# Performance work log

Measured on AMD Instinct MI355X. Metric: run time of the kernel, lower is better.

Reference implementation:

```python
import jax, jax.numpy as jnp
import numpy as np

B = 16384          # batch size
S = 7              # grid size (hard-coded in original)
IMG = 448.0        # image size (hard-coded)
CELL = IMG / S     # 64.0 pixels per cell
LAMBDA_COORD = 5.0
LAMBDA_NOOBJ = 0.5


def setup_inputs() -> dict:
    key = jax.random.key(0)
    k1, k2, k3 = jax.random.split(key, 3)
    # predictions: raw head output [B, 30, 7, 7]; keep >= 0.05 so sqrt(w), sqrt(h) are safe
    input_ = jax.random.uniform(k1, (B, 30, S, S), jnp.float32, 0.05, 1.0)
    # targets already channels-last [B, 7, 7, 30]
    target = jax.random.uniform(k2, (B, S, S, 30), jnp.float32, 0.05, 1.0)
    # objectness channel must be exactly 1.0 where an object exists (code tests == 1)
    conf = (jax.random.uniform(k3, (B, S, S)) < 0.25).astype(jnp.float32)
    target = target.at[..., 4].set(conf)
    return {"input_": input_, "target": target}


def _grid_offsets(dtype):
    # flattened [B*49] pixel offsets of each cell's top-left corner
    g = jnp.arange(S, dtype=dtype)
    gx = jnp.broadcast_to(g[None, :], (S, S)).reshape(-1) * CELL  # varies with column
    gy = jnp.broadcast_to(g[:, None], (S, S)).reshape(-1) * CELL  # varies with row
    return jnp.tile(gx, B), jnp.tile(gy, B)


def _decode_box(p, c, gx, gy):
    # p: [N,30]; box at columns c..c+4 -> clamped corner coords in pixels
    cx = p[:, c] * CELL + gx
    cy = p[:, c + 1] * CELL + gy
    w = p[:, c + 2] * IMG
    h = p[:, c + 3] * IMG
    x1 = jnp.clip(cx - w * 0.5, 0.0, IMG)
    y1 = jnp.clip(cy - h * 0.5, 0.0, IMG)
    x2 = jnp.clip(cx + w * 0.5, 0.0, IMG)
    y2 = jnp.clip(cy + h * 0.5, 0.0, IMG)
    return x1, y1, x2, y2


def _iou(a, b):
    ax1, ay1, ax2, ay2 = a
    bx1, by1, bx2, by2 = b
    l = jnp.maximum(ax1, bx1)
    r = jnp.minimum(ax2, bx2)
    t = jnp.maximum(ay1, by1)
    bo = jnp.minimum(ay2, by2)
    m = (l < r) & (t < bo)
    inter = (r - l) * (bo - t)
    union = (ax2 - ax1) * (ay2 - ay1) + (bx2 - bx1) * (by2 - by1)
    denom = union - inter
    return jnp.where(m, inter / jnp.where(m, denom, 1.0), 0.0)


def _yolo_loss(input_, target):
    # [B,30,7,7] -> [B,7,7,30] -> [N,30]
    x = jnp.transpose(input_, (0, 2, 3, 1)).reshape(-1, 30)
    t = target.reshape(-1, 30)
    gx, gy = _grid_offsets(x.dtype)

    iou1 = _iou(_decode_box(x, 0, gx, gy), _decode_box(t, 0, gx, gy))
    iou2 = _iou(_decode_box(x, 5, gx, gy), _decode_box(t, 5, gx, gy))
    mask = iou1 < iou2                      # True -> second predicted box is responsible
    iou = jnp.where(mask, iou2, iou1)

    sel = jnp.where(mask[:, None], x[:, 5:10], x[:, :5])  # responsible box [N,5]
    w = (t[:, 4] == 1.0).astype(x.dtype)                   # hasObj as 0/1 weights

    coord = jnp.sum(w * ((sel[:, 0] - t[:, 0]) ** 2 + (sel[:, 1] - t[:, 1]) ** 2))
    size = jnp.sum(w * ((jnp.sqrt(sel[:, 2]) - jnp.sqrt(t[:, 2])) ** 2
                        + (jnp.sqrt(sel[:, 3]) - jnp.sqrt(t[:, 3])) ** 2))
    conf = jnp.sum(w * (sel[:, 4] - iou) ** 2)
    noobj = jnp.sum((1.0 - w) * sel[:, 4] ** 2)
    cls = jnp.sum(w[:, None] * (x[:, 10:] - t[:, 10:]) ** 2)

    return (LAMBDA_COORD * coord + LAMBDA_COORD * size + conf
            + LAMBDA_NOOBJ * noobj + cls)


def reference(input_, target):
    return _yolo_loss(input_, target)
```

## Files before the change

kernel.cpp:

```cpp
#include <hip/hip_runtime.h>


#define NCH     30
#define CELLS   49
#define TPB     256
#define WB      6
#define BATCH_F 1470
#define STAGE_F (WB * BATCH_F)
#define STAGE_CHUNKS (STAGE_F / 4)
#define IMGSZ   448.0f
#define CELLSZ  64.0f

__device__ __forceinline__ float iou_f(float ax1, float ay1, float ax2, float ay2,
                                       float bx1, float by1, float bx2, float by2) {
    float l  = fmaxf(ax1, bx1);
    float r  = fminf(ax2, bx2);
    float t  = fmaxf(ay1, by1);
    float bo = fminf(ay2, by2);
    bool  m  = (l < r) && (t < bo);
    float inter = (r - l) * (bo - t);
    float uni   = (ax2 - ax1) * (ay2 - ay1) + (bx2 - bx1) * (by2 - by1);
    float denom = uni - inter;
    return m ? (inter / denom) : 0.0f;
}

__device__ __forceinline__ void decode_box(float p0, float p1, float p2, float p3,
                                           float gx, float gy,
                                           float& x1, float& y1, float& x2, float& y2) {
    float cx = p0 * CELLSZ + gx;
    float cy = p1 * CELLSZ + gy;
    float w  = p2 * IMGSZ;
    float h  = p3 * IMGSZ;
    x1 = fminf(fmaxf(cx - w * 0.5f, 0.0f), IMGSZ);
    y1 = fminf(fmaxf(cy - h * 0.5f, 0.0f), IMGSZ);
    x2 = fminf(fmaxf(cx + w * 0.5f, 0.0f), IMGSZ);
    y2 = fminf(fmaxf(cy + h * 0.5f, 0.0f), IMGSZ);
}

__global__ __launch_bounds__(TPB) void yolo_loss_kernel(
        const float* __restrict__ input,
        const float* __restrict__ target,
        float* __restrict__ out,
        int nbatch) {
    __shared__ __align__(16) float s_in[STAGE_F];
    __shared__ __align__(16) float s_tg[STAGE_F];
    __shared__ float red[TPB / 64];

    const int tid = threadIdx.x;
    const int b0  = blockIdx.x * WB;
    const int nb  = min(WB, nbatch - b0);
    const int nchunks = (nb * BATCH_F) >> 2;

    const float* gin = input  + (long long)b0 * BATCH_F;
    const float* gtg = target + (long long)b0 * BATCH_F;
    #pragma unroll
    for (int k = 0; k < (STAGE_CHUNKS + TPB - 1) / TPB; ++k) {
        int i = k * TPB + tid;
        if (i < nchunks) {
            __builtin_amdgcn_global_load_lds(
                (const __attribute__((address_space(1))) unsigned int*)(gin + i * 4),
                (__attribute__((address_space(3))) unsigned int*)(&s_in[i * 4]),
                16, 0, 0);
            __builtin_amdgcn_global_load_lds(
                (const __attribute__((address_space(1))) unsigned int*)(gtg + i * 4),
                (__attribute__((address_space(3))) unsigned int*)(&s_tg[i * 4]),
                16, 0, 0);
        }
    }
    __syncthreads();

    const int ncell = nb * CELLS;
    float loss = 0.0f;
    for (int local = tid; local < ncell; local += TPB) {
        const int bb  = local / CELLS;
        const int s   = local - bb * CELLS;
        const int row = s / 7;
        const int col = s - row * 7;
        const float gx = (float)col * CELLSZ;
        const float gy = (float)row * CELLSZ;

        const float* __restrict__ tl = &s_tg[local * NCH];
        const float* __restrict__ ipx = &s_in[bb * BATCH_F + s];

        float x[NCH];
        #pragma unroll
        for (int c = 0; c < NCH; ++c) x[c] = ipx[c * CELLS];

        float p0x1, p0y1, p0x2, p0y2, p1x1, p1y1, p1x2, p1y2;
        decode_box(x[0], x[1], x[2], x[3], gx, gy, p0x1, p0y1, p0x2, p0y2);
        decode_box(x[5], x[6], x[7], x[8], gx, gy, p1x1, p1y1, p1x2, p1y2);
        float t0x1, t0y1, t0x2, t0y2, t1x1, t1y1, t1x2, t1y2;
        decode_box(tl[0], tl[1], tl[2], tl[3], gx, gy, t0x1, t0y1, t0x2, t0y2);
        decode_box(tl[5], tl[6], tl[7], tl[8], gx, gy, t1x1, t1y1, t1x2, t1y2);

        float iou1 = iou_f(p0x1, p0y1, p0x2, p0y2, t0x1, t0y1, t0x2, t0y2);
        float iou2 = iou_f(p1x1, p1y1, p1x2, p1y2, t1x1, t1y1, t1x2, t1y2);

        bool  mask = iou1 < iou2;
        float iou  = mask ? iou2 : iou1;
        float s0 = mask ? x[5] : x[0];
        float s1 = mask ? x[6] : x[1];
        float s2 = mask ? x[7] : x[2];
        float s3 = mask ? x[8] : x[3];
        float s4 = mask ? x[9] : x[4];

        float w = (tl[4] == 1.0f) ? 1.0f : 0.0f;

        float d0 = s0 - tl[0];
        float d1 = s1 - tl[1];
        float coord = d0 * d0 + d1 * d1;

        float ds2 = sqrtf(s2) - sqrtf(tl[2]);
        float ds3 = sqrtf(s3) - sqrtf(tl[3]);
        float size = ds2 * ds2 + ds3 * ds3;

        float dc = s4 - iou;
        float conf = dc * dc;
        float noobj = s4 * s4;

        float cls = 0.0f;
        #pragma unroll
        for (int c = 10; c < NCH; ++c) {
            float d = x[c] - tl[c];
            cls += d * d;
        }

        loss += w * (5.0f * (coord + size) + conf + cls) + 0.5f * (1.0f - w) * noobj;
    }

    #pragma unroll
    for (int off = 32; off > 0; off >>= 1)
        loss += __shfl_down(loss, off, 64);

    const int wid  = tid >> 6;
    const int lane = tid & 63;
    if (lane == 0) red[wid] = loss;
    __syncthreads();
    if (tid == 0) {
        float sum = 0.0f;
        #pragma unroll
        for (int i = 0; i < TPB / 64; ++i) sum += red[i];
        atomicAdd(out, sum);
    }
}

extern "C" void kernel_launch(void* const* d_in, const int* in_sizes, int n_in,
                              void* d_out, int out_size, void* d_ws, size_t ws_size,
                              hipStream_t stream) {
    const float* input  = (const float*)d_in[0];
    const float* target = (const float*)d_in[1];
    float* out = (float*)d_out;

    const int nbatch = in_sizes[0] / BATCH_F;
    const int blocks = (nbatch + WB - 1) / WB;

    hipMemsetAsync(d_out, 0, sizeof(float), stream);
    yolo_loss_kernel<<<blocks, TPB, 0, stream>>>(input, target, out, nbatch);
}
```

Measured before the change: 205.6 us.

## Use persistent blocks with double-buffered async LDS staging of batch pairs

Replaces the one-shot staging of six batches per block with 512 persistent blocks that loop over pairs of batches. Each pair is prefetched via global_load_lds into one of two LDS buffers, with explicit vmcnt waits and barriers. This overlaps the global-to-LDS transfer of the next pair with compute on the current one, and cuts the LDS footprint per block. In exchange only 98 threads compute per iteration, each pair costs two barriers, and correctness relies on hand-set waitcnt encodings.

```diff
diff --git a/kernel.cpp b/kernel.cpp
--- a/kernel.cpp
+++ b/kernel.cpp
@@ -4,12 +4,16 @@
 #define NCH     30
 #define CELLS   49
 #define TPB     256
-#define WB      6
+#define NBLK    512
 #define BATCH_F 1470
-#define STAGE_F (WB * BATCH_F)
-#define STAGE_CHUNKS (STAGE_F / 4)
+#define PAIR_F  2940
+#define CHUNKS  735
+#define BUF_F   (2 * PAIR_F)
 #define IMGSZ   448.0f
 #define CELLSZ  64.0f
+
+#define W_VMCNT(n) (((n) & 15) | (0x7 << 4) | (0xF << 8) | ((((n) >> 4) & 3) << 14))
+#define W_LGKM0    (0xF | (0x7 << 4) | (0x0 << 8) | (3 << 14))
 
 __device__ __forceinline__ float iou_f(float ax1, float ay1, float ax2, float ay2,
                                        float bx1, float by1, float bx2, float by2) {
@@ -37,96 +41,126 @@
     y2 = fminf(fmaxf(cy + h * 0.5f, 0.0f), IMGSZ);
 }
 
+__device__ __forceinline__ void issue_pair(const float* __restrict__ input,
+                                           const float* __restrict__ target,
+                                           float* lds_buf, long long pr, int tid) {
+    const float* sin = input  + pr * PAIR_F;
+    const float* stg = target + pr * PAIR_F;
+    #pragma unroll
+    for (int k = 0; k < 3; ++k) {
+        int c = tid + k * TPB;
+        if (c < CHUNKS) {
+            __builtin_amdgcn_global_load_lds(
+                (const __attribute__((address_space(1))) unsigned int*)(sin + c * 4),
+                (__attribute__((address_space(3))) unsigned int*)(lds_buf + c * 4),
+                16, 0, 0);
+        }
+    }
+    #pragma unroll
+    for (int k = 0; k < 3; ++k) {
+        int c = tid + k * TPB;
+        if (c < CHUNKS) {
+            __builtin_amdgcn_global_load_lds(
+                (const __attribute__((address_space(1))) unsigned int*)(stg + c * 4),
+                (__attribute__((address_space(3))) unsigned int*)(lds_buf + PAIR_F + c * 4),
+                16, 0, 0);
+        }
+    }
+}
+
 __global__ __launch_bounds__(TPB) void yolo_loss_kernel(
         const float* __restrict__ input,
         const float* __restrict__ target,
         float* __restrict__ out,
         int nbatch) {
-    __shared__ __align__(16) float s_in[STAGE_F];
-    __shared__ __align__(16) float s_tg[STAGE_F];
+    __shared__ __align__(16) float sbuf[2][BUF_F];
     __shared__ float red[TPB / 64];
 
     const int tid = threadIdx.x;
-    const int b0  = blockIdx.x * WB;
-    const int nb  = min(WB, nbatch - b0);
-    const int nchunks = (nb * BATCH_F) >> 2;
+    const long long npairs = (long long)nbatch >> 1;
+    const long long ppb    = (npairs + NBLK - 1) / NBLK;
+    const long long p0     = (long long)blockIdx.x * ppb;
 
-    const float* gin = input  + (long long)b0 * BATCH_F;
-    const float* gtg = target + (long long)b0 * BATCH_F;
-    #pragma unroll
-    for (int k = 0; k < (STAGE_CHUNKS + TPB - 1) / TPB; ++k) {
-        int i = k * TPB + tid;
-        if (i < nchunks) {
-            __builtin_amdgcn_global_load_lds(
-                (const __attribute__((address_space(1))) unsigned int*)(gin + i * 4),
-                (__attribute__((address_space(3))) unsigned int*)(&s_in[i * 4]),
-                16, 0, 0);
-            __builtin_amdgcn_global_load_lds(
-                (const __attribute__((address_space(1))) unsigned int*)(gtg + i * 4),
-                (__attribute__((address_space(3))) unsigned int*)(&s_tg[i * 4]),
-                16, 0, 0);
-        }
-    }
-    __syncthreads();
+    long long c0 = p0     < npairs ? p0     : npairs - 1;
+    long long c1 = p0 + 1 < npairs ? p0 + 1 : npairs - 1;
+    issue_pair(input, target, sbuf[0], c0, tid);
+    issue_pair(input, target, sbuf[1], c1, tid);
 
-    const int ncell = nb * CELLS;
     float loss = 0.0f;
-    for (int local = tid; local < ncell; local += TPB) {
-        const int bb  = local / CELLS;
-        const int s   = local - bb * CELLS;
-        const int row = s / 7;
-        const int col = s - row * 7;
-        const float gx = (float)col * CELLSZ;
-        const float gy = (float)row * CELLSZ;
+    for (long long j = 0; j < ppb; ++j) {
+        const long long pr = p0 + j;
+        float* buf = sbuf[j & 1];
 
-        const float* __restrict__ tl = &s_tg[local * NCH];
-        const float* __restrict__ ipx = &s_in[bb * BATCH_F + s];
+        __builtin_amdgcn_s_waitcnt(W_VMCNT(6));
+        __builtin_amdgcn_s_barrier();
+        __builtin_amdgcn_sched_barrier(0);
 
-        float x[NCH];
-        #pragma unroll
-        for (int c = 0; c < NCH; ++c) x[c] = ipx[c * CELLS];
+        if (tid < 2 * CELLS && pr < npairs) {
+            const int bb  = tid / CELLS;
+            const int s   = tid - bb * CELLS;
+            const int row = s / 7;
+            const int col = s - row * 7;
+            const float gx = (float)col * CELLSZ;
+            const float gy = (float)row * CELLSZ;
 
-        float p0x1, p0y1, p0x2, p0y2, p1x1, p1y1, p1x2, p1y2;
-        decode_box(x[0], x[1], x[2], x[3], gx, gy, p0x1, p0y1, p0x2, p0y2);
-        decode_box(x[5], x[6], x[7], x[8], gx, gy, p1x1, p1y1, p1x2, p1y2);
-        float t0x1, t0y1, t0x2, t0y2, t1x1, t1y1, t1x2, t1y2;
-        decode_box(tl[0], tl[1], tl[2], tl[3], gx, gy, t0x1, t0y1, t0x2, t0y2);
-        decode_box(tl[5], tl[6], tl[7], tl[8], gx, gy, t1x1, t1y1, t1x2, t1y2);
+            const float* __restrict__ ipx = buf + bb * BATCH_F + s;
+            const float* __restrict__ tl  = buf + PAIR_F + tid * NCH;
 
-        float iou1 = iou_f(p0x1, p0y1, p0x2, p0y2, t0x1, t0y1, t0x2, t0y2);
-        float iou2 = iou_f(p1x1, p1y1, p1x2, p1y2, t1x1, t1y1, t1x2, t1y2);
+            float x[NCH];
+            #pragma unroll
+            for (int c = 0; c < NCH; ++c) x[c] = ipx[c * CELLS];
 
-        bool  mask = iou1 < iou2;
-        float iou  = mask ? iou2 : iou1;
-        float s0 = mask ? x[5] : x[0];
-        float s1 = mask ? x[6] : x[1];
-        float s2 = mask ? x[7] : x[2];
-        float s3 = mask ? x[8] : x[3];
-        float s4 = mask ? x[9] : x[4];
+            float p0x1, p0y1, p0x2, p0y2, p1x1, p1y1, p1x2, p1y2;
+            decode_box(x[0], x[1], x[2], x[3], gx, gy, p0x1, p0y1, p0x2, p0y2);
+            decode_box(x[5], x[6], x[7], x[8], gx, gy, p1x1, p1y1, p1x2, p1y2);
+            float t0x1, t0y1, t0x2, t0y2, t1x1, t1y1, t1x2, t1y2;
+            decode_box(tl[0], tl[1], tl[2], tl[3], gx, gy, t0x1, t0y1, t0x2, t0y2);
+            decode_box(tl[5], tl[6], tl[7], tl[8], gx, gy, t1x1, t1y1, t1x2, t1y2);
 
-        float w = (tl[4] == 1.0f) ? 1.0f : 0.0f;
+            float iou1 = iou_f(p0x1, p0y1, p0x2, p0y2, t0x1, t0y1, t0x2, t0y2);
+            float iou2 = iou_f(p1x1, p1y1, p1x2, p1y2, t1x1, t1y1, t1x2, t1y2);
 
-        float d0 = s0 - tl[0];
-        float d1 = s1 - tl[1];
-        float coord = d0 * d0 + d1 * d1;
+            bool  mask = iou1 < iou2;
+            float iou  = mask ? iou2 : iou1;
+            float s0 = mask ? x[5] : x[0];
+            float s1 = mask ? x[6] : x[1];
+            float s2 = mask ? x[7] : x[2];
+            float s3 = mask ? x[8] : x[3];
+            float s4 = mask ? x[9] : x[4];
 
-        float ds2 = sqrtf(s2) - sqrtf(tl[2]);
-        float ds3 = sqrtf(s3) - sqrtf(tl[3]);
-        float size = ds2 * ds2 + ds3 * ds3;
+            float w = (tl[4] == 1.0f) ? 1.0f : 0.0f;
 
-        float dc = s4 - iou;
-        float conf = dc * dc;
-        float noobj = s4 * s4;
+            float d0 = s0 - tl[0];
+            float d1 = s1 - tl[1];
+            float coord = d0 * d0 + d1 * d1;
 
-        float cls = 0.0f;
-        #pragma unroll
-        for (int c = 10; c < NCH; ++c) {
-            float d = x[c] - tl[c];
-            cls += d * d;
+            float ds2 = sqrtf(s2) - sqrtf(tl[2]);
+            float ds3 = sqrtf(s3) - sqrtf(tl[3]);
+            float size = ds2 * ds2 + ds3 * ds3;
+
+            float dc = s4 - iou;
+            float conf = dc * dc;
+            float noobj = s4 * s4;
+
+            float cls = 0.0f;
+            #pragma unroll
+            for (int c = 10; c < NCH; ++c) {
+                float d = x[c] - tl[c];
+                cls += d * d;
+            }
+
+            loss += w * (5.0f * (coord + size) + conf + cls) + 0.5f * (1.0f - w) * noobj;
         }
 
-        loss += w * (5.0f * (coord + size) + conf + cls) + 0.5f * (1.0f - w) * noobj;
+        __builtin_amdgcn_s_waitcnt(W_LGKM0);
+        __builtin_amdgcn_sched_barrier(0);
+        __builtin_amdgcn_s_barrier();
+
+        long long pn = pr + 2 < npairs ? pr + 2 : npairs - 1;
+        issue_pair(input, target, buf, pn, tid);
     }
+
+    __builtin_amdgcn_s_waitcnt(W_VMCNT(0));
 
     #pragma unroll
     for (int off = 32; off > 0; off >>= 1)
@@ -137,10 +171,10 @@
     if (lane == 0) red[wid] = loss;
     __syncthreads();
     if (tid == 0) {
-        float sum = 0.0f;
+        float s = 0.0f;
         #pragma unroll
-        for (int i = 0; i < TPB / 64; ++i) sum += red[i];
-        atomicAdd(out, sum);
+        for (int i = 0; i < TPB / 64; ++i) s += red[i];
+        atomicAdd(out, s);
     }
 }
 
@@ -152,8 +186,6 @@
     float* out = (float*)d_out;
 
     const int nbatch = in_sizes[0] / BATCH_F;
-    const int blocks = (nbatch + WB - 1) / WB;
-
     hipMemsetAsync(d_out, 0, sizeof(float), stream);
-    yolo_loss_kernel<<<blocks, TPB, 0, stream>>>(input, target, out, nbatch);
+    yolo_loss_kernel<<<NBLK, TPB, 0, stream>>>(input, target, out, nbatch);
 }
```

After: 213.2 us. 1.04x slower.
